# Kernel optimization log

Measured on AMD Instinct MI355X. Metric: run time of the kernel, lower is better.

Reference implementation:

```python
import jax, jax.numpy as jnp
import numpy as np


def setup_inputs() -> dict:
    key = jax.random.key(0)
    k1, k2 = jax.random.split(key)
    z = jax.random.normal(k1, (16, 256, 32, 32), dtype=jnp.float32)
    emb = jax.random.normal(k2, (8192, 256), dtype=jnp.float32)
    return {"z": z, "emb": emb}


def reference(z, emb):
    B, C, H, W = z.shape
    # [B,C,H,W] -> [B*H*W, C], distances in fp32 for precision
    z_f = jnp.transpose(z, (0, 2, 3, 1)).reshape(-1, C).astype(jnp.float32)
    e = emb.astype(jnp.float32)
    # squared-distance expansion: ||z||^2 - 2 z.e + ||e||^2  -> [N, K]
    d = (
        jnp.sum(z_f * z_f, axis=1, keepdims=True)
        - 2.0 * (z_f @ e.T)
        + jnp.sum(e * e, axis=1)[None, :]
    )
    idx = jnp.argmin(d, axis=1)  # [N]
    out = emb[idx].astype(z.dtype)  # codebook gather
    return jnp.transpose(out.reshape(B, H, W, C), (0, 3, 1, 2))
```

## Files before the change

### kernel.cpp

```cpp
#include <hip/hip_runtime.h>
#include <stdint.h>

#define NB   16
#define CD   256
#define HW   1024
#define NQ   16384
#define KCN  8192

typedef unsigned long long u64;
typedef unsigned short     u16;
using f32x4  = __attribute__((ext_vector_type(4))) float;
using bf16x8 = __attribute__((ext_vector_type(8))) __bf16;

#define ZTB_OFF  0
#define EMBB_OFF 8388608
#define EH_OFF   12582912
#define CAND_OFF 12615680

static __device__ __forceinline__ void gl_lds16(const void* g, void* l) {
  __builtin_amdgcn_global_load_lds(
      (const __attribute__((address_space(1))) void*)g,
      (__attribute__((address_space(3))) void*)l, 16, 0, 0);
}

static __device__ __forceinline__ unsigned bf16r(float x) {
  unsigned u = __float_as_uint(x);
  return (u + 0x7fffu + ((u >> 16) & 1u)) >> 16;
}

static __device__ __forceinline__ u64 umin64(u64 a, u64 b) { return a < b ? a : b; }
static __device__ __forceinline__ u64 umax64(u64 a, u64 b) { return a < b ? b : a; }

__global__ __launch_bounds__(256) void k_prep(const float* __restrict__ z,
                                              const float* __restrict__ emb,
                                              u16* __restrict__ zTb,
                                              u16* __restrict__ embB,
                                              float* __restrict__ eH) {
  const int bx = (int)blockIdx.x;
  if (bx < 1024) {
    __shared__ float tile[64][65];
    const int b   = bx >> 6;
    const int hwT = (bx >> 2) & 15;
    const int cT  = bx & 3;
    const int tx  = threadIdx.x & 63;
    const int ty  = threadIdx.x >> 6;
    const float* src = z + (size_t)(b * CD + cT * 64) * HW + hwT * 64;
#pragma unroll
    for (int i = 0; i < 16; ++i) {
      const int c_l = ty + 4 * i;
      tile[c_l][tx] = src[(size_t)c_l * HW + tx];
    }
    __syncthreads();
    const size_t dbase = (size_t)(b * HW + hwT * 64) * CD + cT * 64;
    const int rsub = tx >> 4;
    const int cq   = (tx & 15) * 4;
#pragma unroll
    for (int i = 0; i < 4; ++i) {
      const int r = ty * 16 + i * 4 + rsub;
      ushort4 pk;
      pk.x = (u16)bf16r(tile[cq + 0][r]);
      pk.y = (u16)bf16r(tile[cq + 1][r]);
      pk.z = (u16)bf16r(tile[cq + 2][r]);
      pk.w = (u16)bf16r(tile[cq + 3][r]);
      *(ushort4*)(zTb + dbase + (size_t)r * CD + cq) = pk;
    }
  } else {
    const int wave = (bx - 1024) * 4 + ((int)threadIdx.x >> 6);
    const int lane = threadIdx.x & 63;
#pragma unroll
    for (int it = 0; it < 8; ++it) {
      const int row = wave * 8 + it;
      const float4 v = *(const float4*)(emb + (size_t)row * CD + lane * 4);
      uint2 pk;
      pk.x = bf16r(v.x) | (bf16r(v.y) << 16);
      pk.y = bf16r(v.z) | (bf16r(v.w) << 16);
      *(uint2*)(embB + (size_t)row * CD + lane * 4) = pk;
      float s = v.x * v.x + v.y * v.y + v.z * v.z + v.w * v.w;
#pragma unroll
      for (int off = 32; off; off >>= 1) s += __shfl_xor(s, off, 64);
      if (lane == 0) eH[row] = 0.5f * s + 1024.0f;
    }
  }
}


#define WAITV(N) asm volatile("s_waitcnt vmcnt(" #N ")" ::: "memory")
#define MEMFENCE() asm volatile("" ::: "memory")

__global__ __launch_bounds__(256, 2) void k_argmin(const u16* __restrict__ zTb,
                                                   const u16* __restrict__ embB,
                                                   const float* __restrict__ eH,
                                                   u64* __restrict__ cand) {
  __shared__ __align__(16) u16 Bs[4][128 * 64];

  const int tid  = (int)threadIdx.x;
  const int w    = tid >> 6;
  const int lane = tid & 63;
  const int l15  = lane & 15, quad = lane >> 4;
  const int q0    = (int)(blockIdx.x >> 3) * 128;
  const int split = (int)(blockIdx.x & 7);

  bf16x8 Af[2][4][2];
  {
    const char* aB = (const char*)zTb
                   + ((size_t)(q0 + w * 32 + l15) * CD + quad * 8) * 2;
#pragma unroll
    for (int i = 0; i < 2; ++i)
#pragma unroll
      for (int kc = 0; kc < 4; ++kc)
#pragma unroll
        for (int ks = 0; ks < 2; ++ks)
          Af[i][kc][ks] = *(const bf16x8*)(aB + i * 8192 + kc * 128 + ks * 64);
  }
  MEMFENCE();

  const char* bS = (const char*)embB + (size_t)split * (1024 * 512)
                 + (size_t)(w * 32 + (lane >> 3)) * 512
                 + (size_t)(((lane & 7) ^ (lane >> 3)) * 16);
  const int ldsW = w * 4096 + lane * 16;

#define STAGE(RING, NT_, KC_)                                                  \
  do {                                                                         \
    const char* _s = bS + (NT_) * 65536 + (KC_) * 128;                         \
    char* _d = (char*)Bs[RING] + ldsW;                                         \
    gl_lds16(_s,         _d);                                                  \
    gl_lds16(_s + 4096,  _d + 1024);                                           \
    gl_lds16(_s + 8192,  _d + 2048);                                           \
    gl_lds16(_s + 12288, _d + 3072);                                           \
  } while (0)

  const int bR0 = l15 * 128 + ((quad ^ (l15 & 7)) * 16);
  const int bR1 = bR0 ^ 64;

  f32x4 acc[2][8];
  float b1[8][2], b2[8][2];
  const float FMAX = __uint_as_float(0x7F7FFFFFu);
#pragma unroll
  for (int s = 0; s < 8; ++s) { b1[s][0] = b1[s][1] = FMAX; b2[s][0] = b2[s][1] = FMAX; }

  STAGE(0, 0, 0); MEMFENCE();
  STAGE(1, 0, 1); MEMFENCE();
  STAGE(2, 0, 2); MEMFENCE();

#define MFMA_INT(RING, KC_)                                                    \
  do {                                                                         \
    const char* _b = (const char*)Bs[RING];                                    \
    _Pragma("unroll")                                                          \
    for (int ks = 0; ks < 2; ++ks) {                                           \
      bf16x8 bfr[8];                                                           \
      const int _o = ks ? bR1 : bR0;                                           \
      _Pragma("unroll")                                                        \
      for (int j = 0; j < 8; ++j)                                              \
        bfr[j] = *(const bf16x8*)(_b + j * 2048 + _o);                         \
      __builtin_amdgcn_s_setprio(1);                                           \
      _Pragma("unroll")                                                        \
      for (int i = 0; i < 2; ++i)                                              \
        _Pragma("unroll")                                                      \
        for (int j = 0; j < 8; ++j)                                            \
          acc[i][j] = __builtin_amdgcn_mfma_f32_16x16x32_bf16(                 \
              Af[i][KC_][ks], bfr[j], acc[i][j], 0, 0, 0);                     \
      __builtin_amdgcn_s_setprio(0);                                           \
    }                                                                          \
  } while (0)

#define EPILOGUE(NT_)                                                          \
  do {                                                                         \
    _Pragma("unroll")                                                          \
    for (int i = 0; i < 2; ++i)                                                \
      _Pragma("unroll")                                                        \
      for (int r = 0; r < 4; ++r) {                                            \
        const int s = i * 4 + r;                                               \
        float kq[8];                                                           \
        _Pragma("unroll")                                                      \
        for (int j = 0; j < 8; ++j)                                            \
          kq[j] = __uint_as_float(                                             \
              (__float_as_uint(eh[j] - acc[i][j][r]) & ~63u)                   \
              | (unsigned)((NT_) * 8 + j));                                    \
        _Pragma("unroll")                                                      \
        for (int h = 0; h < 2; ++h) {                                          \
          const float k0 = kq[4 * h], k1 = kq[4 * h + 1];                      \
          const float k2 = kq[4 * h + 2], k3 = kq[4 * h + 3];                  \
          const float lo01 = fminf(k0, k1), hi01 = fmaxf(k0, k1);              \
          const float lo23 = fminf(k2, k3), hi23 = fmaxf(k2, k3);              \
          const float best = fminf(lo01, lo23);                                \
          const float sec  = fminf(fmaxf(lo01, lo23), fminf(hi01, hi23));      \
          b2[s][h] = fminf(fmaxf(best, b1[s][h]), fminf(sec, b2[s][h]));       \
          b1[s][h] = fminf(best, b1[s][h]);                                    \
        }                                                                      \
      }                                                                        \
  } while (0)

  float eh[8];

  for (int nt = 0; nt < 7; ++nt) {
    const int n0 = split * 1024 + nt * 128;
#pragma unroll
    for (int i = 0; i < 2; ++i)
#pragma unroll
      for (int j = 0; j < 8; ++j) acc[i][j] = f32x4{0.f, 0.f, 0.f, 0.f};

    WAITV(8); __builtin_amdgcn_s_barrier(); MEMFENCE();
    STAGE(3, nt, 3); MEMFENCE();
#pragma unroll
    for (int j = 0; j < 8; ++j) eh[j] = eH[n0 + j * 16 + l15];
    MEMFENCE();
    MFMA_INT(0, 0);
    WAITV(16); __builtin_amdgcn_s_barrier(); MEMFENCE();
    STAGE(0, nt + 1, 0); MEMFENCE();
    MFMA_INT(1, 1);
    WAITV(16); __builtin_amdgcn_s_barrier(); MEMFENCE();
    STAGE(1, nt + 1, 1); MEMFENCE();
    MFMA_INT(2, 2);
    WAITV(16); __builtin_amdgcn_s_barrier(); MEMFENCE();
    STAGE(2, nt + 1, 2); MEMFENCE();
    MFMA_INT(3, 3);

    EPILOGUE(nt);
  }

  {
    const int n0 = split * 1024 + 7 * 128;
#pragma unroll
    for (int i = 0; i < 2; ++i)
#pragma unroll
      for (int j = 0; j < 8; ++j) acc[i][j] = f32x4{0.f, 0.f, 0.f, 0.f};

    WAITV(8); __builtin_amdgcn_s_barrier(); MEMFENCE();
    STAGE(3, 7, 3); MEMFENCE();
#pragma unroll
    for (int j = 0; j < 8; ++j) eh[j] = eH[n0 + j * 16 + l15];
    MEMFENCE();
    MFMA_INT(0, 0);

    WAITV(16); __builtin_amdgcn_s_barrier(); MEMFENCE();
    MFMA_INT(1, 1);

    WAITV(12); __builtin_amdgcn_s_barrier(); MEMFENCE();
    MFMA_INT(2, 2);

    WAITV(8); __builtin_amdgcn_s_barrier(); MEMFENCE();
    MFMA_INT(3, 3);

    EPILOGUE(7);
  }
#undef STAGE
#undef MFMA_INT
#undef EPILOGUE

#pragma unroll
  for (int s = 0; s < 8; ++s) {
#pragma unroll
    for (int h = 0; h < 2; ++h) {
      u64 x1 = ((u64)__float_as_uint(b1[s][h]) << 32) | (unsigned)l15;
      u64 x2 = ((u64)__float_as_uint(b2[s][h]) << 32) | (unsigned)l15;
#pragma unroll
      for (int off = 1; off < 16; off <<= 1) {
        const u64 o1 = __shfl_xor(x1, off, 64);
        const u64 o2 = __shfl_xor(x2, off, 64);
        const u64 lo = umin64(x1, o1);
        const u64 hi = umax64(x1, o1);
        x1 = lo;
        x2 = umin64(hi, umin64(x2, o2));
      }
      if (l15 == 0) {
        const int i = s >> 2, r = s & 3;
        const int q = q0 + w * 32 + i * 16 + quad * 4 + r;
        const unsigned kb1 = (unsigned)(x1 >> 32), kb2 = (unsigned)(x2 >> 32);
        const int n1 = split * 1024 + (int)((kb1 >> 3) & 7) * 128
                       + (int)(kb1 & 7) * 16 + (int)(x1 & 15);
        const int n2 = split * 1024 + (int)((kb2 >> 3) & 7) * 128
                       + (int)(kb2 & 7) * 16 + (int)(x2 & 15);
        cand[(size_t)q * 32 + split * 4 + h * 2 + 0] = ((u64)kb1 << 32) | (unsigned)n1;
        cand[(size_t)q * 32 + split * 4 + h * 2 + 1] = ((u64)kb2 << 32) | (unsigned)n2;
      }
    }
  }
}

__global__ __launch_bounds__(1024) void k_pick_out(const float* __restrict__ z,
                                                   const float* __restrict__ emb,
                                                   const u64* __restrict__ cand,
                                                   float* __restrict__ out) {
  __shared__ float zs[256][66];
  const int t    = (int)threadIdx.x;
  const int lane = t & 63;
  const int wv   = t >> 6;
  const int l15  = t & 15;
  const int g    = t >> 4;
  const int q0b  = (int)blockIdx.x * 64;
  const int b    = q0b >> 10, hw0 = q0b & 1023;

  {
    const int hw   = (lane & 31) * 2;
    const int csub = lane >> 5;
#pragma unroll
    for (int i = 0; i < 8; ++i) {
      const int c = wv * 16 + i * 2 + csub;
      const float2 v = *(const float2*)(z + ((size_t)(b * CD + c)) * HW + hw0 + hw);
      *(float2*)&zs[c][hw] = v;
    }
  }
  __syncthreads();

  const int q = q0b + g;
  const u64* cp = cand + (size_t)q * 32 + l15 * 2;
  const u64 v0 = cp[0], v1 = cp[1];
  u64 s0 = umin64(v0, v1), s1 = umax64(v0, v1), s2 = ~0ull, s3 = ~0ull;
#pragma unroll
  for (int off = 1; off < 16; off <<= 1) {
    const u64 b0 = __shfl_xor(s0, off, 64);
    const u64 b1 = __shfl_xor(s1, off, 64);
    const u64 b2 = __shfl_xor(s2, off, 64);
    const u64 b3 = __shfl_xor(s3, off, 64);
    const u64 c0 = umin64(s0, b0);
    const u64 c1 = umin64(umin64(s1, b1), umax64(s0, b0));
    const u64 c2 = umin64(umin64(s2, b2),
                          umin64(umax64(s1, b0), umax64(s0, b1)));
    const u64 c3 = umin64(umin64(umin64(s3, b3), umax64(s2, b0)),
                          umin64(umax64(s0, b2), umax64(s1, b1)));
    s0 = c0; s1 = c1; s2 = c2; s3 = c3;
  }
  const u64 sel[4] = {s0, s1, s2, s3};

  float zq[16];
#pragma unroll
  for (int j = 0; j < 16; ++j) zq[j] = zs[j * 16 + l15][g];

  double bd = 1e300;
  int bi = 0x7fffffff;
#pragma unroll
  for (int c4 = 0; c4 < 4; ++c4) {
    const int idx = (int)(unsigned)(sel[c4] & 0xffffffffull);
    const float* er = emb + (size_t)idx * CD;
    double s = 0.0;
#pragma unroll
    for (int j = 0; j < 16; ++j) {
      const double d = (double)zq[j] - (double)er[j * 16 + l15];
      s += d * d;
    }
#pragma unroll
    for (int off = 1; off < 16; off <<= 1) s += __shfl_xor(s, off, 64);
    const bool better = (s < bd) || (s == bd && idx < bi);
    if (better) { bd = s; bi = idx; }
  }

  __syncthreads();
  {
    const float* ew = emb + (size_t)bi * CD;
#pragma unroll
    for (int j = 0; j < 16; ++j) zs[j * 16 + l15][g] = ew[j * 16 + l15];
  }
  __syncthreads();
  {
    const int hw   = (lane & 31) * 2;
    const int csub = lane >> 5;
#pragma unroll
    for (int i = 0; i < 8; ++i) {
      const int c = wv * 16 + i * 2 + csub;
      const float2 v = *(const float2*)&zs[c][hw];
      *(float2*)(out + ((size_t)(b * CD + c)) * HW + hw0 + hw) = v;
    }
  }
}

extern "C" void kernel_launch(void* const* d_in, const int* in_sizes, int n_in,
                              void* d_out, int out_size, void* d_ws, size_t ws_size,
                              hipStream_t stream) {
  const float* z   = (const float*)d_in[0];
  const float* emb = (const float*)d_in[1];
  float* out = (float*)d_out;

  char* ws = (char*)d_ws;
  u16*   zTb  = (u16*)(ws + ZTB_OFF);
  u16*   embB = (u16*)(ws + EMBB_OFF);
  float* eH   = (float*)(ws + EH_OFF);
  u64*   cand = (u64*)(ws + CAND_OFF);

  k_prep<<<1280, 256, 0, stream>>>(z, emb, zTb, embB, eH);
  k_argmin<<<1024, 256, 0, stream>>>(zTb, embB, eH, cand);
  k_pick_out<<<256, 1024, 0, stream>>>(z, emb, cand, out);
}
```

Baseline: 172.1 us.

## Split argmin block into 8 waves halving codebook columns per wave, triple-buffer LDS

The argmin kernel now runs 512 threads per block. Two wave groups share the same 128 queries and each handles half of every 128-column codebook tile, so each wave holds half the accumulators and candidate state. The LDS ring shrinks from four to three buffers with rotating pointers, and each thread issues two async loads per stage instead of four. The aim is lower register pressure and higher occupancy (launch bounds 512,6) to hide latency, at the cost of reloading the A fragments in both wave groups and repacking the candidate index into fewer tag bits.

```diff
diff --git a/kernel.cpp b/kernel.cpp
--- a/kernel.cpp
+++ b/kernel.cpp
@@ -87,11 +87,11 @@
 #define WAITV(N) asm volatile("s_waitcnt vmcnt(" #N ")" ::: "memory")
 #define MEMFENCE() asm volatile("" ::: "memory")
 
-__global__ __launch_bounds__(256, 2) void k_argmin(const u16* __restrict__ zTb,
+__global__ __launch_bounds__(512, 6) void k_argmin(const u16* __restrict__ zTb,
                                                    const u16* __restrict__ embB,
                                                    const float* __restrict__ eH,
                                                    u64* __restrict__ cand) {
-  __shared__ __align__(16) u16 Bs[4][128 * 64];
+  __shared__ __align__(16) u16 Bs[3][128 * 64];
 
   const int tid  = (int)threadIdx.x;
   const int w    = tid >> 6;
@@ -99,11 +99,12 @@
   const int l15  = lane & 15, quad = lane >> 4;
   const int q0    = (int)(blockIdx.x >> 3) * 128;
   const int split = (int)(blockIdx.x & 7);
+  const int qg = w & 3;
+  const int nh = w >> 2;
 
   bf16x8 Af[2][4][2];
   {
-    const char* aB = (const char*)zTb
-                   + ((size_t)(q0 + w * 32 + l15) * CD + quad * 8) * 2;
+    const char* aB = (const char*)zTb + (size_t)(q0 + qg * 32 + l15) * 512 + quad * 16;
 #pragma unroll
     for (int i = 0; i < 2; ++i)
 #pragma unroll
@@ -114,49 +115,51 @@
   }
   MEMFENCE();
 
-  const char* bS = (const char*)embB + (size_t)split * (1024 * 512)
-                 + (size_t)(w * 32 + (lane >> 3)) * 512
-                 + (size_t)(((lane & 7) ^ (lane >> 3)) * 16);
-  const int ldsW = w * 4096 + lane * 16;
-
-#define STAGE(RING, NT_, KC_)                                                  \
+  const char* bS = (const char*)embB + (size_t)split * 524288
+                 + (size_t)(tid >> 3) * 512
+                 + (size_t)(((tid & 7) ^ ((tid >> 3) & 7)) * 16);
+  const int ldsW = tid * 16;
+
+#define STAGEP(P_, NT_, KC_)                                                   \
   do {                                                                         \
     const char* _s = bS + (NT_) * 65536 + (KC_) * 128;                         \
-    char* _d = (char*)Bs[RING] + ldsW;                                         \
+    char* _d = (char*)(P_) + ldsW;                                             \
     gl_lds16(_s,         _d);                                                  \
-    gl_lds16(_s + 4096,  _d + 1024);                                           \
-    gl_lds16(_s + 8192,  _d + 2048);                                           \
-    gl_lds16(_s + 12288, _d + 3072);                                           \
+    gl_lds16(_s + 32768, _d + 8192);                                           \
+    MEMFENCE();                                                                \
   } while (0)
 
-  const int bR0 = l15 * 128 + ((quad ^ (l15 & 7)) * 16);
+  const int bR0 = (nh * 64 + l15) * 128 + ((quad ^ (l15 & 7)) * 16);
   const int bR1 = bR0 ^ 64;
 
-  f32x4 acc[2][8];
-  float b1[8][2], b2[8][2];
+  f32x4 acc[2][4];
+  float b1[8], b2[8];
   const float FMAX = __uint_as_float(0x7F7FFFFFu);
 #pragma unroll
-  for (int s = 0; s < 8; ++s) { b1[s][0] = b1[s][1] = FMAX; b2[s][0] = b2[s][1] = FMAX; }
-
-  STAGE(0, 0, 0); MEMFENCE();
-  STAGE(1, 0, 1); MEMFENCE();
-  STAGE(2, 0, 2); MEMFENCE();
-
-#define MFMA_INT(RING, KC_)                                                    \
+  for (int s = 0; s < 8; ++s) { b1[s] = FMAX; b2[s] = FMAX; }
+
+  char* p0 = (char*)Bs[0];
+  char* p1 = (char*)Bs[1];
+  char* p2 = (char*)Bs[2];
+
+  STAGEP(p0, 0, 0);
+  STAGEP(p1, 0, 1);
+
+#define MFMA_P(P_, KC_)                                                        \
   do {                                                                         \
-    const char* _b = (const char*)Bs[RING];                                    \
+    const char* _b = (const char*)(P_);                                        \
     _Pragma("unroll")                                                          \
     for (int ks = 0; ks < 2; ++ks) {                                           \
-      bf16x8 bfr[8];                                                           \
+      bf16x8 bfr[4];                                                           \
       const int _o = ks ? bR1 : bR0;                                           \
       _Pragma("unroll")                                                        \
-      for (int j = 0; j < 8; ++j)                                              \
+      for (int j = 0; j < 4; ++j)                                              \
         bfr[j] = *(const bf16x8*)(_b + j * 2048 + _o);                         \
       __builtin_amdgcn_s_setprio(1);                                           \
       _Pragma("unroll")                                                        \
       for (int i = 0; i < 2; ++i)                                              \
         _Pragma("unroll")                                                      \
-        for (int j = 0; j < 8; ++j)                                            \
+        for (int j = 0; j < 4; ++j)                                            \
           acc[i][j] = __builtin_amdgcn_mfma_f32_16x16x32_bf16(                 \
               Af[i][KC_][ks], bfr[j], acc[i][j], 0, 0, 0);                     \
       __builtin_amdgcn_s_setprio(0);                                           \
@@ -170,109 +173,107 @@
       _Pragma("unroll")                                                        \
       for (int r = 0; r < 4; ++r) {                                            \
         const int s = i * 4 + r;                                               \
-        float kq[8];                                                           \
+        float kq[4];                                                           \
         _Pragma("unroll")                                                      \
-        for (int j = 0; j < 8; ++j)                                            \
+        for (int j = 0; j < 4; ++j)                                            \
           kq[j] = __uint_as_float(                                             \
-              (__float_as_uint(eh[j] - acc[i][j][r]) & ~63u)                   \
-              | (unsigned)((NT_) * 8 + j));                                    \
-        _Pragma("unroll")                                                      \
-        for (int h = 0; h < 2; ++h) {                                          \
-          const float k0 = kq[4 * h], k1 = kq[4 * h + 1];                      \
-          const float k2 = kq[4 * h + 2], k3 = kq[4 * h + 3];                  \
-          const float lo01 = fminf(k0, k1), hi01 = fmaxf(k0, k1);              \
-          const float lo23 = fminf(k2, k3), hi23 = fmaxf(k2, k3);              \
-          const float best = fminf(lo01, lo23);                                \
-          const float sec  = fminf(fmaxf(lo01, lo23), fminf(hi01, hi23));      \
-          b2[s][h] = fminf(fmaxf(best, b1[s][h]), fminf(sec, b2[s][h]));       \
-          b1[s][h] = fminf(best, b1[s][h]);                                    \
-        }                                                                      \
+              (__float_as_uint(eh[j] - acc[i][j][r]) & ~31u)                   \
+              | (unsigned)((NT_) * 4 + j));                                    \
+        const float lo01 = fminf(kq[0], kq[1]), hi01 = fmaxf(kq[0], kq[1]);    \
+        const float lo23 = fminf(kq[2], kq[3]), hi23 = fmaxf(kq[2], kq[3]);    \
+        const float best = fminf(lo01, lo23);                                  \
+        const float sec  = fminf(fmaxf(lo01, lo23), fminf(hi01, hi23));        \
+        b2[s] = fminf(fmaxf(best, b1[s]), fminf(sec, b2[s]));                  \
+        b1[s] = fminf(best, b1[s]);                                            \
       }                                                                        \
   } while (0)
 
-  float eh[8];
+  float eh[4];
+  const float* ehP = eH + split * 1024 + nh * 64 + l15;
 
   for (int nt = 0; nt < 7; ++nt) {
-    const int n0 = split * 1024 + nt * 128;
 #pragma unroll
     for (int i = 0; i < 2; ++i)
 #pragma unroll
-      for (int j = 0; j < 8; ++j) acc[i][j] = f32x4{0.f, 0.f, 0.f, 0.f};
-
-    WAITV(8); __builtin_amdgcn_s_barrier(); MEMFENCE();
-    STAGE(3, nt, 3); MEMFENCE();
-#pragma unroll
-    for (int j = 0; j < 8; ++j) eh[j] = eH[n0 + j * 16 + l15];
+      for (int j = 0; j < 4; ++j) acc[i][j] = f32x4{0.f, 0.f, 0.f, 0.f};
+
+    WAITV(2); __builtin_amdgcn_s_barrier(); MEMFENCE();
+    STAGEP(p2, nt, 2);
+#pragma unroll
+    for (int j = 0; j < 4; ++j) eh[j] = ehP[nt * 128 + j * 16];
     MEMFENCE();
-    MFMA_INT(0, 0);
-    WAITV(16); __builtin_amdgcn_s_barrier(); MEMFENCE();
-    STAGE(0, nt + 1, 0); MEMFENCE();
-    MFMA_INT(1, 1);
-    WAITV(16); __builtin_amdgcn_s_barrier(); MEMFENCE();
-    STAGE(1, nt + 1, 1); MEMFENCE();
-    MFMA_INT(2, 2);
-    WAITV(16); __builtin_amdgcn_s_barrier(); MEMFENCE();
-    STAGE(2, nt + 1, 2); MEMFENCE();
-    MFMA_INT(3, 3);
+    MFMA_P(p0, 0);
+
+    WAITV(6); __builtin_amdgcn_s_barrier(); MEMFENCE();
+    STAGEP(p0, nt, 3);
+    MFMA_P(p1, 1);
+
+    WAITV(6); __builtin_amdgcn_s_barrier(); MEMFENCE();
+    STAGEP(p1, nt + 1, 0);
+    MFMA_P(p2, 2);
+
+    WAITV(2); __builtin_amdgcn_s_barrier(); MEMFENCE();
+    STAGEP(p2, nt + 1, 1);
+    MFMA_P(p0, 3);
 
     EPILOGUE(nt);
-  }
-
-  {
-    const int n0 = split * 1024 + 7 * 128;
+
+    char* tmp = p0; p0 = p1; p1 = p2; p2 = tmp;
+  }
+
+  {
 #pragma unroll
     for (int i = 0; i < 2; ++i)
 #pragma unroll
-      for (int j = 0; j < 8; ++j) acc[i][j] = f32x4{0.f, 0.f, 0.f, 0.f};
-
-    WAITV(8); __builtin_amdgcn_s_barrier(); MEMFENCE();
-    STAGE(3, 7, 3); MEMFENCE();
-#pragma unroll
-    for (int j = 0; j < 8; ++j) eh[j] = eH[n0 + j * 16 + l15];
+      for (int j = 0; j < 4; ++j) acc[i][j] = f32x4{0.f, 0.f, 0.f, 0.f};
+
+    WAITV(2); __builtin_amdgcn_s_barrier(); MEMFENCE();
+    STAGEP(p2, 7, 2);
+#pragma unroll
+    for (int j = 0; j < 4; ++j) eh[j] = ehP[7 * 128 + j * 16];
     MEMFENCE();
-    MFMA_INT(0, 0);
-
-    WAITV(16); __builtin_amdgcn_s_barrier(); MEMFENCE();
-    MFMA_INT(1, 1);
-
-    WAITV(12); __builtin_amdgcn_s_barrier(); MEMFENCE();
-    MFMA_INT(2, 2);
-
-    WAITV(8); __builtin_amdgcn_s_barrier(); MEMFENCE();
-    MFMA_INT(3, 3);
+    MFMA_P(p0, 0);
+
+    WAITV(6); __builtin_amdgcn_s_barrier(); MEMFENCE();
+    STAGEP(p0, 7, 3);
+    MFMA_P(p1, 1);
+
+    WAITV(6); __builtin_amdgcn_s_barrier(); MEMFENCE();
+    MFMA_P(p2, 2);
+
+    WAITV(0); __builtin_amdgcn_s_barrier(); MEMFENCE();
+    MFMA_P(p0, 3);
 
     EPILOGUE(7);
   }
-#undef STAGE
-#undef MFMA_INT
+#undef STAGEP
+#undef MFMA_P
 #undef EPILOGUE
 
 #pragma unroll
   for (int s = 0; s < 8; ++s) {
-#pragma unroll
-    for (int h = 0; h < 2; ++h) {
-      u64 x1 = ((u64)__float_as_uint(b1[s][h]) << 32) | (unsigned)l15;
-      u64 x2 = ((u64)__float_as_uint(b2[s][h]) << 32) | (unsigned)l15;
-#pragma unroll
-      for (int off = 1; off < 16; off <<= 1) {
-        const u64 o1 = __shfl_xor(x1, off, 64);
-        const u64 o2 = __shfl_xor(x2, off, 64);
-        const u64 lo = umin64(x1, o1);
-        const u64 hi = umax64(x1, o1);
-        x1 = lo;
-        x2 = umin64(hi, umin64(x2, o2));
-      }
-      if (l15 == 0) {
-        const int i = s >> 2, r = s & 3;
-        const int q = q0 + w * 32 + i * 16 + quad * 4 + r;
-        const unsigned kb1 = (unsigned)(x1 >> 32), kb2 = (unsigned)(x2 >> 32);
-        const int n1 = split * 1024 + (int)((kb1 >> 3) & 7) * 128
-                       + (int)(kb1 & 7) * 16 + (int)(x1 & 15);
-        const int n2 = split * 1024 + (int)((kb2 >> 3) & 7) * 128
-                       + (int)(kb2 & 7) * 16 + (int)(x2 & 15);
-        cand[(size_t)q * 32 + split * 4 + h * 2 + 0] = ((u64)kb1 << 32) | (unsigned)n1;
-        cand[(size_t)q * 32 + split * 4 + h * 2 + 1] = ((u64)kb2 << 32) | (unsigned)n2;
-      }
+    u64 x1 = ((u64)__float_as_uint(b1[s]) << 32) | (unsigned)l15;
+    u64 x2 = ((u64)__float_as_uint(b2[s]) << 32) | (unsigned)l15;
+#pragma unroll
+    for (int off = 1; off < 16; off <<= 1) {
+      const u64 o1 = __shfl_xor(x1, off, 64);
+      const u64 o2 = __shfl_xor(x2, off, 64);
+      const u64 lo = umin64(x1, o1);
+      const u64 hi = umax64(x1, o1);
+      x1 = lo;
+      x2 = umin64(hi, umin64(x2, o2));
+    }
+    if (l15 == 0) {
+      const int i = s >> 2, r = s & 3;
+      const int q = q0 + qg * 32 + i * 16 + quad * 4 + r;
+      const unsigned kb1 = (unsigned)(x1 >> 32), kb2 = (unsigned)(x2 >> 32);
+      const int id1 = (int)(kb1 & 31u), id2 = (int)(kb2 & 31u);
+      const int n1 = split * 1024 + (id1 >> 2) * 128 + nh * 64
+                     + (id1 & 3) * 16 + (int)(x1 & 15);
+      const int n2 = split * 1024 + (id2 >> 2) * 128 + nh * 64
+                     + (id2 & 3) * 16 + (int)(x2 & 15);
+      cand[(size_t)q * 32 + split * 4 + nh * 2 + 0] = ((u64)kb1 << 32) | (unsigned)n1;
+      cand[(size_t)q * 32 + split * 4 + nh * 2 + 1] = ((u64)kb2 << 32) | (unsigned)n2;
     }
   }
 }
@@ -377,6 +378,6 @@
   u64*   cand = (u64*)(ws + CAND_OFF);
 
   k_prep<<<1280, 256, 0, stream>>>(z, emb, zTb, embB, eH);
-  k_argmin<<<1024, 256, 0, stream>>>(zTb, embB, eH, cand);
+  k_argmin<<<1024, 512, 0, stream>>>(zTb, embB, eH, cand);
   k_pick_out<<<256, 1024, 0, stream>>>(z, emb, cand, out);
 }
```

After: 354.8 us. 2.06x slower.
